# Performance work log

Hardware: AMD Instinct MI355X
Metric: run time of the kernel (lower is better)

The kernel has to match this reference:

```python
import jax, jax.numpy as jnp
import numpy as np

N_EMBD = 1024
N_HEAD = 16
HEAD_DIM = N_EMBD / N_HEAD  # used only for the attention scale, as in the source
LN_EPS = 1e-5


def _layernorm(x, g, b):
    mu = jnp.mean(x, axis=-1, keepdims=True)
    var = jnp.mean(jnp.square(x - mu), axis=-1, keepdims=True)
    return (x - mu) * jax.lax.rsqrt(var + LN_EPS) * g + b


def setup_inputs() -> dict:
    key = jax.random.key(0)
    ks = jax.random.split(key, 8)
    D = N_EMBD
    s = lambda n: 0.02  # GPT-style init scale
    x = jax.random.normal(ks[0], (4, 2048, D), dtype=jnp.float32)
    w_attn = jax.random.normal(ks[1], (D, 3 * D), dtype=jnp.float32) * s(D)
    b_attn = jnp.zeros((3 * D,), jnp.float32)
    w_proj = jax.random.normal(ks[2], (D, D), dtype=jnp.float32) * s(D)
    b_proj = jnp.zeros((D,), jnp.float32)
    ln1_g = jnp.ones((D,), jnp.float32)
    ln1_b = jnp.zeros((D,), jnp.float32)
    ln2_g = jnp.ones((D,), jnp.float32)
    ln2_b = jnp.zeros((D,), jnp.float32)
    w_fc = jax.random.normal(ks[3], (D, 4 * D), dtype=jnp.float32) * s(D)
    b_fc = jnp.zeros((4 * D,), jnp.float32)
    w_fc2 = jax.random.normal(ks[4], (4 * D, D), dtype=jnp.float32) * s(4 * D)
    b_fc2 = jnp.zeros((D,), jnp.float32)
    return {"x": x, "w_attn": w_attn, "b_attn": b_attn, "w_proj": w_proj,
            "b_proj": b_proj, "ln1_g": ln1_g, "ln1_b": ln1_b, "ln2_g": ln2_g,
            "ln2_b": ln2_b, "w_fc": w_fc, "b_fc": b_fc, "w_fc2": w_fc2,
            "b_fc2": b_fc2}


def reference(x, w_attn, b_attn, w_proj, b_proj, ln1_g, ln1_b, ln2_g, ln2_b,
              w_fc, b_fc, w_fc2, b_fc2):
    B, T, D = x.shape
    # --- attention branch (pre-LN) ---
    h = _layernorm(x, ln1_g, ln1_b)
    qkv = h @ w_attn + b_attn                     # [B,T,3D]
    q, k, v = jnp.split(qkv, 3, axis=-1)
    scale = 1.0 / np.sqrt(HEAD_DIM).astype(np.float32)
    att = jnp.einsum('btd,bsd->bts', q, k) * scale  # full-dim scores [B,T,T]
    causal = jnp.tril(jnp.ones((T, T), dtype=bool))
    att = jnp.where(causal[None, :, :], att, -jnp.inf)
    att = jax.nn.softmax(att, axis=-1)
    y = jnp.einsum('bts,bsd->btd', att, v)
    y = y @ w_proj + b_proj
    x = x + y
    # --- MLP branch (pre-LN) ---
    h = _layernorm(x, ln2_g, ln2_b)
    h = jax.nn.gelu(h @ w_fc + b_fc, approximate=True)
    h = h @ w_fc2 + b_fc2
    return x + h
```

## Files before the change

kernel.cpp:

```cpp
#include <hip/hip_runtime.h>
#include <math.h>


typedef unsigned short u16;
typedef __attribute__((ext_vector_type(8))) short bf16x8;
typedef __attribute__((ext_vector_type(8))) unsigned short u16x8;
typedef __attribute__((ext_vector_type(4))) float f32x4;

#define DEV __device__ __forceinline__

#define GLOAD_LDS16(gp, lp)                                                     \
    __builtin_amdgcn_global_load_lds(                                           \
        (const __attribute__((address_space(1))) void*)(gp),                    \
        (__attribute__((address_space(3))) void*)(lp), 16, 0, 0)

DEV float bf2f(u16 h) {
    union { unsigned u; float f; } t; t.u = ((unsigned)h) << 16; return t.f;
}
DEV u16 f2bf(float f) {
    union { unsigned u; float f; } t; t.f = f;
    unsigned u = t.u;
    return (u16)((u + 0x7FFFu + ((u >> 16) & 1u)) >> 16);
}
DEV float loadIn(const void* p, long i, int isbf) {
    return isbf ? bf2f(((const u16*)p)[i]) : ((const float*)p)[i];
}
DEV float gelu_fast(float x) {
    float u = 1.5957691216057308f * (x + 0.044715f * x * x * x);
    return x * __builtin_amdgcn_rcpf(1.0f + __expf(-u));
}

DEV float waveSum(float v) {
    #pragma unroll
    for (int o = 32; o > 0; o >>= 1) v += __shfl_down(v, o, 64);
    return v;
}
DEV float waveMax(float v) {
    #pragma unroll
    for (int o = 32; o > 0; o >>= 1) v = fmaxf(v, __shfl_down(v, o, 64));
    return v;
}

template <bool IS_MAX>
DEV float blockReduce(float v) {
    __shared__ float tmp[5];
    __syncthreads();
    v = IS_MAX ? waveMax(v) : waveSum(v);
    int lane = threadIdx.x & 63, w = threadIdx.x >> 6;
    if (lane == 0) tmp[w] = v;
    __syncthreads();
    if (threadIdx.x == 0) {
        float r = tmp[0];
        for (int i = 1; i < 4; i++) r = IS_MAX ? fmaxf(r, tmp[i]) : (r + tmp[i]);
        tmp[4] = r;
    }
    __syncthreads();
    return tmp[4];
}

__global__ void detect_dtype(const u16* __restrict__ xr, int* __restrict__ flag) {
    const int tid = threadIdx.x;
    int cnt = 0;
    #pragma unroll
    for (int i = 0; i < 16; i++) {
        unsigned u = xr[2 * (tid + 256 * i)];
        unsigned e = (u >> 7) & 0xFF;
        cnt += (e >= 100 && e <= 140) ? 1 : 0;
    }
    __shared__ int sh[4];
    #pragma unroll
    for (int o = 32; o > 0; o >>= 1) cnt += __shfl_down(cnt, o, 64);
    if ((tid & 63) == 0) sh[tid >> 6] = cnt;
    __syncthreads();
    if (tid == 0) flag[0] = (sh[0] + sh[1] + sh[2] + sh[3] > 2048) ? 1 : 0;
}

template <bool RAW_IN>
__global__ void ln_kernel(const void* __restrict__ x, const void* __restrict__ g,
                          const void* __restrict__ b, u16* __restrict__ out,
                          const int* __restrict__ flagp) {
    const int isbf = *flagp;
    const int inbf = RAW_IN ? isbf : 1;
    const long base = (long)blockIdx.x * 1024;
    const int tid = threadIdx.x;
    float v[4];
    #pragma unroll
    for (int j = 0; j < 4; j++) v[j] = loadIn(x, base + tid + 256 * j, inbf);
    float mu = blockReduce<false>(v[0] + v[1] + v[2] + v[3]) * (1.0f / 1024.0f);
    float d[4], sq = 0.f;
    #pragma unroll
    for (int j = 0; j < 4; j++) { d[j] = v[j] - mu; sq += d[j] * d[j]; }
    float var = blockReduce<false>(sq) * (1.0f / 1024.0f);
    float rstd = rsqrtf(var + 1e-5f);
    #pragma unroll
    for (int j = 0; j < 4; j++) {
        int c = tid + 256 * j;
        out[base + c] = f2bf(d[j] * rstd * loadIn(g, c, isbf) + loadIn(b, c, isbf));
    }
}

__global__ void transpose_to_bf16(const void* __restrict__ in, int ldin, long inBatch,
                                  u16* __restrict__ out, int ldout, long outBatch,
                                  const int* __restrict__ flagp) {
    __shared__ u16 tile[32][33];
    const int isbf = flagp ? *flagp : 1;
    const long ibase = (long)blockIdx.z * inBatch;
    out += (long)blockIdx.z * outBatch;
    const int bc = blockIdx.x * 32, br = blockIdx.y * 32;
    const int tx = threadIdx.x & 31, ty = threadIdx.x >> 5;
    #pragma unroll
    for (int i = 0; i < 32; i += 8)
        tile[ty + i][tx] = f2bf(loadIn(in, ibase + (long)(br + ty + i) * ldin + bc + tx, isbf));
    __syncthreads();
    #pragma unroll
    for (int i = 0; i < 32; i += 8)
        out[(long)(bc + ty + i) * ldout + br + tx] = tile[tx][ty + i];
}

template <int MODE, int CAUSAL, int TM>
__global__ __launch_bounds__(256) void gemm_mf(
        const u16* __restrict__ A, int lda, long aBatch,
        const u16* __restrict__ Bt, int ldb, long bBatch,
        const void* __restrict__ bias,
        void* __restrict__ Cv, int ldc, long cBatch,
        const void* __restrict__ res,
        float scale, const int* __restrict__ flagp, int K) {
    constexpr int FI = TM / 32;
    const int m0 = blockIdx.y * TM, n0 = blockIdx.x * 128;
    if (CAUSAL == 1 && n0 > m0 + TM - 1) return;
    __shared__ __align__(16) u16 sA[TM * 32];
    __shared__ __align__(16) u16 sB[128 * 32];
    const int bz = blockIdx.z;
    A  += (long)bz * aBatch + (long)m0 * lda;
    Bt += (long)bz * bBatch + (long)n0 * ldb;
    const int tid = threadIdx.x;
    const int wave = tid >> 6, lane = tid & 63;
    const int quad = lane >> 4, l16 = lane & 15;
    const int wr = (wave >> 1) * (TM / 2), wc = (wave & 1) * 64;

    const int c0 = tid;
    const int r0 = c0 >> 2;
    const int qs = (c0 & 3) ^ ((r0 >> 1) & 3);
    const u16* ag = A  + (long)r0 * lda + qs * 8;
    const u16* bg = Bt + (long)r0 * ldb + qs * 8;
    u16* sAd = sA + c0 * 8;
    u16* sBd = sB + c0 * 8;
    const long aStep = (long)64 * lda, bStep = (long)64 * ldb;

    f32x4 acc[FI][4];
    #pragma unroll
    for (int i = 0; i < FI; i++)
        #pragma unroll
        for (int j = 0; j < 4; j++)
            acc[i][j] = f32x4{0.f, 0.f, 0.f, 0.f};

    int Keff = K;
    if (CAUSAL == 2) Keff = min(K, m0 + TM);

    const int qa = quad ^ ((l16 >> 1) & 3);

    for (int k0 = 0; k0 < Keff; k0 += 32) {
        __syncthreads();
        GLOAD_LDS16(ag + k0, sAd);
        if (TM == 128) GLOAD_LDS16(ag + k0 + aStep, sAd + 2048);
        GLOAD_LDS16(bg + k0,         sBd);
        GLOAD_LDS16(bg + k0 + bStep, sBd + 2048);
        __syncthreads();
        bf16x8 af[FI], bfv[4];
        #pragma unroll
        for (int i = 0; i < FI; i++)
            af[i]  = *reinterpret_cast<const bf16x8*>(&sA[(wr + 16 * i + l16) * 32 + qa * 8]);
        #pragma unroll
        for (int j = 0; j < 4; j++)
            bfv[j] = *reinterpret_cast<const bf16x8*>(&sB[(wc + 16 * j + l16) * 32 + qa * 8]);
        #pragma unroll
        for (int i = 0; i < FI; i++)
            #pragma unroll
            for (int j = 0; j < 4; j++)
                acc[i][j] = __builtin_amdgcn_mfma_f32_16x16x32_bf16(
                    af[i], bfv[j], acc[i][j], 0, 0, 0);
    }

    const int isbf = (MODE == 0 || MODE == 3 || MODE == 4 || MODE == 5) ? *flagp : 1;
    #pragma unroll
    for (int i = 0; i < FI; i++) {
        #pragma unroll
        for (int j = 0; j < 4; j++) {
            #pragma unroll
            for (int r = 0; r < 4; r++) {
                const int row = m0 + wr + 16 * i + quad * 4 + r;
                const int col = n0 + wc + 16 * j + l16;
                const long idx = (long)bz * cBatch + (long)row * ldc + col;
                float v = acc[i][j][r];
                if (MODE == 1) {
                    reinterpret_cast<u16*>(Cv)[idx] = f2bf(v * scale);
                } else {
                    if (MODE != 2) v += loadIn(bias, col, isbf);
                    if (MODE == 4) v = gelu_fast(v);
                    if (MODE == 3) v += loadIn(res, (long)row * ldc + col, isbf);
                    if (MODE == 5) v += bf2f(((const u16*)res)[(long)row * ldc + col]);
                    if (MODE == 5 && !isbf)
                        reinterpret_cast<float*>(Cv)[idx] = v;
                    else
                        reinterpret_cast<u16*>(Cv)[idx] = f2bf(v);
                }
            }
        }
    }
}

__global__ void softmax_causal(const u16* __restrict__ S, u16* __restrict__ P) {
    const long row = blockIdx.x;
    const int t = (int)(row & 2047);
    const u16* sr = S + row * 2048;
    u16* pr = P + row * 2048;
    const int tid = threadIdx.x;
    const int s0 = tid * 8;
    float v[8];
    float mx = -INFINITY;
    if (s0 <= t) {
        u16x8 raw = *reinterpret_cast<const u16x8*>(sr + s0);
        #pragma unroll
        for (int i = 0; i < 8; i++) {
            float x = bf2f(raw[i]);
            v[i] = (s0 + i <= t) ? x : -INFINITY;
            mx = fmaxf(mx, v[i]);
        }
    } else {
        #pragma unroll
        for (int i = 0; i < 8; i++) v[i] = -INFINITY;
    }
    mx = blockReduce<true>(mx);
    float sum = 0.f;
    #pragma unroll
    for (int i = 0; i < 8; i++) {
        float e = (v[i] == -INFINITY) ? 0.0f : __expf(v[i] - mx);
        v[i] = e;
        sum += e;
    }
    sum = blockReduce<false>(sum);
    float inv = 1.0f / sum;
    if (s0 <= (t | 63)) {
        u16x8 o;
        #pragma unroll
        for (int i = 0; i < 8; i++) o[i] = f2bf(v[i] * inv);
        *reinterpret_cast<u16x8*>(pr + s0) = o;
    }
}

extern "C" void kernel_launch(void* const* d_in, const int* in_sizes, int n_in,
                              void* d_out, int out_size, void* d_ws, size_t ws_size,
                              hipStream_t stream) {
    const void* x      = d_in[0];
    const void* w_attn = d_in[1];
    const void* b_attn = d_in[2];
    const void* w_proj = d_in[3];
    const void* b_proj = d_in[4];
    const void* ln1_g  = d_in[5];
    const void* ln1_b  = d_in[6];
    const void* ln2_g  = d_in[7];
    const void* ln2_b  = d_in[8];
    const void* w_fc   = d_in[9];
    const void* b_fc   = d_in[10];
    const void* w_fc2  = d_in[11];
    const void* b_fc2  = d_in[12];

    char* ws = (char*)d_ws;
    u16*   hbuf   = (u16*)(ws);
    u16*   qkv    = (u16*)(ws + 16777216);
    u16*   S      = (u16*)(ws + 67108864);
    u16*   wattnT = (u16*)(ws + 134217728);
    u16*   wprojT = wattnT + 3072 * 1024;
    u16*   wfcT   = wprojT + 1024 * 1024;
    u16*   wfc2T  = wfcT + 4096 * 1024;
    u16*   vT     = wfc2T + 1024 * 4096;
    int*   flag   = (int*)(ws + 176160768);
    u16*   probs  = qkv;
    u16*   x1     = qkv + 16777216;

    detect_dtype<<<1, 256, 0, stream>>>((const u16*)x, flag);

    transpose_to_bf16<<<dim3(96, 32, 1),  256, 0, stream>>>(w_attn, 3072, 0, wattnT, 1024, 0, flag);
    transpose_to_bf16<<<dim3(32, 32, 1),  256, 0, stream>>>(w_proj, 1024, 0, wprojT, 1024, 0, flag);
    transpose_to_bf16<<<dim3(128, 32, 1), 256, 0, stream>>>(w_fc,   4096, 0, wfcT,   1024, 0, flag);
    transpose_to_bf16<<<dim3(32, 128, 1), 256, 0, stream>>>(w_fc2,  1024, 0, wfc2T,  4096, 0, flag);

    ln_kernel<true><<<8192, 256, 0, stream>>>(x, ln1_g, ln1_b, hbuf, flag);

    gemm_mf<0, 0, 128><<<dim3(24, 64, 1), 256, 0, stream>>>(
        hbuf, 1024, 0, wattnT, 1024, 0, b_attn, qkv, 3072, 0, nullptr, 0.f, flag, 1024);

    transpose_to_bf16<<<dim3(32, 64, 4), 256, 0, stream>>>(
        qkv + 2048, 3072, (long)2048 * 3072, vT, 2048, (long)1024 * 2048, nullptr);

    gemm_mf<1, 1, 64><<<dim3(16, 32, 4), 256, 0, stream>>>(
        qkv, 3072, (long)2048 * 3072, qkv + 1024, 3072, (long)2048 * 3072,
        nullptr, S, 2048, (long)2048 * 2048, nullptr, 0.125f, flag, 1024);

    softmax_causal<<<8192, 256, 0, stream>>>(S, probs);

    gemm_mf<2, 2, 64><<<dim3(8, 32, 4), 256, 0, stream>>>(
        probs, 2048, (long)2048 * 2048, vT, 2048, (long)1024 * 2048,
        nullptr, hbuf, 1024, (long)2048 * 1024, nullptr, 0.f, flag, 2048);

    gemm_mf<3, 0, 64><<<dim3(8, 128, 1), 256, 0, stream>>>(
        hbuf, 1024, 0, wprojT, 1024, 0, b_proj, x1, 1024, 0, x, 0.f, flag, 1024);

    ln_kernel<false><<<8192, 256, 0, stream>>>(x1, ln2_g, ln2_b, hbuf, flag);

    gemm_mf<4, 0, 128><<<dim3(32, 64, 1), 256, 0, stream>>>(
        hbuf, 1024, 0, wfcT, 1024, 0, b_fc, S, 4096, 0, nullptr, 0.f, flag, 1024);

    gemm_mf<5, 0, 128><<<dim3(8, 64, 1), 256, 0, stream>>>(
        S, 4096, 0, wfc2T, 4096, 0, b_fc2, d_out, 1024, 0, x1, 0.f, flag, 4096);
}
```

Baseline: 689.0 us.

## Add 256x256-tile 8-wave pipelined GEMM for QKV and MLP projections

Introduces a new bf16 MFMA GEMM kernel with 256x256 output tiles, 512 threads (8 waves), XOR-swizzled LDS, double-buffered direct global-to-LDS loads split into four phases interleaved with compute, and an XCD-aware block swizzle. It replaces the previous 128-tile GEMM for the QKV, FC and FC2 projections, aiming at more data reuse per tile and overlap of loads with MFMA work. The cost is larger LDS use (128 KB per block) and heavy register pressure from 32 accumulators per thread. Grids are also much smaller (e.g. 128 blocks for FC2), which may leave part of the GPU idle.

After: 696.6 us. About the same (+1.1%).

```diff
diff --git a/kernel.cpp b/kernel.cpp
--- a/kernel.cpp
+++ b/kernel.cpp
@@ -209,6 +209,138 @@
     }
 }
 
+template <int MODE>
+__global__ __launch_bounds__(512, 2) void gemm_8ph(
+        const u16* __restrict__ A, int lda,
+        const u16* __restrict__ Bt, int ldb,
+        const void* __restrict__ bias,
+        void* __restrict__ Cv, int ldc,
+        const void* __restrict__ res,
+        const int* __restrict__ flagp, int K) {
+    __shared__ __align__(16) u16 sA[2][256 * 64];
+    __shared__ __align__(16) u16 sB[2][256 * 64];
+
+    const int gx  = gridDim.x;
+    const int nwg = gx * gridDim.y;
+    const int fid = blockIdx.y * gx + blockIdx.x;
+    const int swz = (fid & 7) * (nwg >> 3) + (fid >> 3);
+    const int m0 = (swz / gx) * 256, n0 = (swz % gx) * 256;
+
+    const int tid  = threadIdx.x;
+    const int lane = tid & 63, wv = tid >> 6;
+    const int wm = wv >> 2, wn = wv & 3;
+    const int l16 = lane & 15, quad = lane >> 4;
+    const int xg = l16 & 7;
+
+    const int rq   = tid >> 3;
+    const int gsrc = ((tid & 7) ^ (rq & 7)) * 8;
+    const int gdst = (tid & 7) * 8;
+    const int rAb  = (rq < 32) ? rq : 96 + rq;
+
+    const int NT = K >> 6;
+
+#define STAGE8(t_, q_) do {                                                      \
+        const int sl_ = (t_) & 1;                                                \
+        const int k0_ = (t_) << 6;                                               \
+        const int ra_ = ((q_) << 5) + rAb;                                       \
+        GLOAD_LDS16(A + (long)(m0 + ra_) * lda + k0_ + gsrc,                     \
+                    &sA[sl_][ra_ * 64 + gdst]);                                  \
+        const int rb_ = ((q_) << 6) + rq;                                        \
+        GLOAD_LDS16(Bt + (long)(n0 + rb_) * ldb + k0_ + gsrc,                    \
+                    &sB[sl_][rb_ * 64 + gdst]);                                  \
+    } while (0)
+
+#define PBAR8() do { __builtin_amdgcn_sched_barrier(0);                          \
+        asm volatile("s_barrier" ::: "memory");                                  \
+        __builtin_amdgcn_sched_barrier(0); } while (0)
+
+#define WVM8(n_) do { __builtin_amdgcn_sched_barrier(0);                         \
+        asm volatile("s_waitcnt vmcnt(" #n_ ")" ::: "memory");                   \
+        __builtin_amdgcn_sched_barrier(0); } while (0)
+
+    f32x4 acc[8][4];
+    #pragma unroll
+    for (int i = 0; i < 8; i++)
+        #pragma unroll
+        for (int j = 0; j < 4; j++) acc[i][j] = f32x4{0.f, 0.f, 0.f, 0.f};
+
+    STAGE8(0, 0); STAGE8(0, 1); STAGE8(0, 2); STAGE8(0, 3);
+    WVM8(4);
+    STAGE8(1, 0); STAGE8(1, 1); STAGE8(1, 2);
+    WVM8(6);
+    PBAR8();
+
+    for (int u = 0; u < NT; ++u) {
+        const int su = u & 1;
+        bf16x8 bfr[4][2];
+        #pragma unroll
+        for (int q = 0; q < 4; ++q) {
+            bf16x8 af[2][2];
+            #pragma unroll
+            for (int f = 0; f < 2; ++f)
+                #pragma unroll
+                for (int s = 0; s < 2; ++s)
+                    af[f][s] = *reinterpret_cast<const bf16x8*>(
+                        &sA[su][(wm * 128 + (2 * q + f) * 16 + l16) * 64 +
+                                (((s * 4 + quad) ^ xg) * 8)]);
+            if (q == 0) {
+                #pragma unroll
+                for (int j = 0; j < 4; ++j)
+                    #pragma unroll
+                    for (int s = 0; s < 2; ++s)
+                        bfr[j][s] = *reinterpret_cast<const bf16x8*>(
+                            &sB[su][(wn * 64 + j * 16 + l16) * 64 +
+                                    (((s * 4 + quad) ^ xg) * 8)]);
+            }
+            if (q == 0) { if (u + 1 < NT) STAGE8(u + 1, 3); }
+            else        { if (u + 2 < NT) STAGE8(u + 2, q - 1); }
+            PBAR8();
+            __builtin_amdgcn_s_setprio(1);
+            #pragma unroll
+            for (int f = 0; f < 2; ++f)
+                #pragma unroll
+                for (int j = 0; j < 4; ++j) {
+                    acc[2 * q + f][j] = __builtin_amdgcn_mfma_f32_16x16x32_bf16(
+                        af[f][0], bfr[j][0], acc[2 * q + f][j], 0, 0, 0);
+                    acc[2 * q + f][j] = __builtin_amdgcn_mfma_f32_16x16x32_bf16(
+                        af[f][1], bfr[j][1], acc[2 * q + f][j], 0, 0, 0);
+                }
+            __builtin_amdgcn_s_setprio(0);
+            if (q < 3) {
+                PBAR8();
+            } else if (u + 1 < NT) {
+                if (u + 2 < NT) { WVM8(6); } else { WVM8(0); }
+                PBAR8();
+            }
+        }
+    }
+
+    const int isbf = *flagp;
+    #pragma unroll
+    for (int mi = 0; mi < 8; ++mi) {
+        #pragma unroll
+        for (int j = 0; j < 4; ++j) {
+            #pragma unroll
+            for (int r = 0; r < 4; ++r) {
+                const int row = m0 + wm * 128 + mi * 16 + quad * 4 + r;
+                const int col = n0 + wn * 64 + j * 16 + l16;
+                const long idx = (long)row * ldc + col;
+                float v = acc[mi][j][r];
+                v += loadIn(bias, col, isbf);
+                if (MODE == 4) v = gelu_fast(v);
+                if (MODE == 5) v += bf2f(((const u16*)res)[idx]);
+                if (MODE == 5 && !isbf)
+                    reinterpret_cast<float*>(Cv)[idx] = v;
+                else
+                    reinterpret_cast<u16*>(Cv)[idx] = f2bf(v);
+            }
+        }
+    }
+#undef STAGE8
+#undef PBAR8
+#undef WVM8
+}
+
 __global__ void softmax_causal(const u16* __restrict__ S, u16* __restrict__ P) {
     const long row = blockIdx.x;
     const int t = (int)(row & 2047);
@@ -287,8 +419,8 @@
 
     ln_kernel<true><<<8192, 256, 0, stream>>>(x, ln1_g, ln1_b, hbuf, flag);
 
-    gemm_mf<0, 0, 128><<<dim3(24, 64, 1), 256, 0, stream>>>(
-        hbuf, 1024, 0, wattnT, 1024, 0, b_attn, qkv, 3072, 0, nullptr, 0.f, flag, 1024);
+    gemm_8ph<0><<<dim3(12, 32, 1), 512, 0, stream>>>(
+        hbuf, 1024, wattnT, 1024, b_attn, qkv, 3072, nullptr, flag, 1024);
 
     transpose_to_bf16<<<dim3(32, 64, 4), 256, 0, stream>>>(
         qkv + 2048, 3072, (long)2048 * 3072, vT, 2048, (long)1024 * 2048, nullptr);
@@ -308,9 +440,9 @@
 
     ln_kernel<false><<<8192, 256, 0, stream>>>(x1, ln2_g, ln2_b, hbuf, flag);
 
-    gemm_mf<4, 0, 128><<<dim3(32, 64, 1), 256, 0, stream>>>(
-        hbuf, 1024, 0, wfcT, 1024, 0, b_fc, S, 4096, 0, nullptr, 0.f, flag, 1024);
-
-    gemm_mf<5, 0, 128><<<dim3(8, 64, 1), 256, 0, stream>>>(
-        S, 4096, 0, wfc2T, 4096, 0, b_fc2, d_out, 1024, 0, x1, 0.f, flag, 4096);
-}
+    gemm_8ph<4><<<dim3(16, 32, 1), 512, 0, stream>>>(
+        hbuf, 1024, wfcT, 1024, b_fc, S, 4096, nullptr, flag, 1024);
+
+    gemm_8ph<5><<<dim3(4, 32, 1), 512, 0, stream>>>(
+        S, 4096, wfc2T, 4096, b_fc2, d_out, 1024, x1, flag, 4096);
+}
```

## Replace GEMM with 256x256 double-buffered eight-phase pipelined MFMA kernel

Applied to the files above, without the earlier changes.

Swaps the simple 128/64-row tile GEMM for a 512-thread kernel using 256x256 tiles and BK=64. Global-to-LDS loads are double-buffered and split into four quarter stages, interleaved with MFMA phases through explicit waitcnt and barriers. The kernel also adds a triangular block enumeration for the causal score GEMM and an XCD-style block swizzle for the dense GEMMs. Softmax zero-fill is widened to 256 columns to match the larger causal tile. The aim is more data reuse and overlap of memory with MFMA work. The cost is much higher register and LDS use, fewer blocks for the smaller GEMMs, and more causal waste per tile.

Result: no change. 686.5 us (-0.4%).

```diff
diff --git a/kernel.cpp b/kernel.cpp
--- a/kernel.cpp
+++ b/kernel.cpp
@@ -13,6 +13,12 @@
     __builtin_amdgcn_global_load_lds(                                           \
         (const __attribute__((address_space(1))) void*)(gp),                    \
         (__attribute__((address_space(3))) void*)(lp), 16, 0, 0)
+
+#define DSR128(dst_, p_)                                                        \
+    asm volatile("ds_read_b128 %0, %1"                                          \
+                 : "=v"(dst_)                                                   \
+                 : "v"((unsigned)(unsigned long long)                           \
+                       (__attribute__((address_space(3))) const void*)(p_)))
 
 DEV float bf2f(u16 h) {
     union { unsigned u; float f; } t; t.u = ((unsigned)h) << 16; return t.f;
@@ -117,85 +123,174 @@
         out[(long)(bc + ty + i) * ldout + br + tx] = tile[tx][ty + i];
 }
 
-template <int MODE, int CAUSAL, int TM>
-__global__ __launch_bounds__(256) void gemm_mf(
+template <int MODE, int CAUSAL>
+__global__ __launch_bounds__(512, 2) void gemm_8ph(
         const u16* __restrict__ A, int lda, long aBatch,
         const u16* __restrict__ Bt, int ldb, long bBatch,
         const void* __restrict__ bias,
         void* __restrict__ Cv, int ldc, long cBatch,
         const void* __restrict__ res,
         float scale, const int* __restrict__ flagp, int K) {
-    constexpr int FI = TM / 32;
-    const int m0 = blockIdx.y * TM, n0 = blockIdx.x * 128;
-    if (CAUSAL == 1 && n0 > m0 + TM - 1) return;
-    __shared__ __align__(16) u16 sA[TM * 32];
-    __shared__ __align__(16) u16 sB[128 * 32];
+    __shared__ __align__(16) u16 sA[2][256 * 64];
+    __shared__ __align__(16) u16 sB[2][256 * 64];
+
+    int m0, n0;
+    if (CAUSAL == 1) {
+        const int bx = blockIdx.x;
+        int ti = (int)((sqrtf(8.0f * bx + 1.0f) - 1.0f) * 0.5f);
+        while ((ti + 1) * (ti + 2) / 2 <= bx) ++ti;
+        while (ti * (ti + 1) / 2 > bx) --ti;
+        m0 = ti * 256;
+        n0 = (bx - ti * (ti + 1) / 2) * 256;
+    } else if (CAUSAL == 2) {
+        m0 = blockIdx.y * 256;
+        n0 = blockIdx.x * 256;
+    } else {
+        const int gx  = gridDim.x;
+        const int nwg = gx * gridDim.y;
+        const int fid = blockIdx.y * gx + blockIdx.x;
+        const int swz = (fid & 7) * (nwg >> 3) + (fid >> 3);
+        m0 = (swz / gx) * 256;
+        n0 = (swz % gx) * 256;
+    }
     const int bz = blockIdx.z;
-    A  += (long)bz * aBatch + (long)m0 * lda;
-    Bt += (long)bz * bBatch + (long)n0 * ldb;
-    const int tid = threadIdx.x;
-    const int wave = tid >> 6, lane = tid & 63;
-    const int quad = lane >> 4, l16 = lane & 15;
-    const int wr = (wave >> 1) * (TM / 2), wc = (wave & 1) * 64;
-
-    const int c0 = tid;
-    const int r0 = c0 >> 2;
-    const int qs = (c0 & 3) ^ ((r0 >> 1) & 3);
-    const u16* ag = A  + (long)r0 * lda + qs * 8;
-    const u16* bg = Bt + (long)r0 * ldb + qs * 8;
-    u16* sAd = sA + c0 * 8;
-    u16* sBd = sB + c0 * 8;
-    const long aStep = (long)64 * lda, bStep = (long)64 * ldb;
-
-    f32x4 acc[FI][4];
-    #pragma unroll
-    for (int i = 0; i < FI; i++)
+    A  += (long)bz * aBatch;
+    Bt += (long)bz * bBatch;
+
+    const int tid  = threadIdx.x;
+    const int lane = tid & 63, wv = tid >> 6;
+    const int wm = wv >> 2, wn = wv & 3;
+    const int l16 = lane & 15, quad = lane >> 4;
+    const int xg = l16 & 7;
+
+    const int rq   = tid >> 3;
+    const int gsrc = ((tid & 7) ^ (rq & 7)) * 8;
+    const int gdst = (tid & 7) * 8;
+    const int rAb  = (rq < 32) ? rq : 96 + rq;
+
+    int NT = K >> 6;
+    if (CAUSAL == 2) NT = min(K, m0 + 256) >> 6;
+
+#define STAGE8(t_, q_) do {                                                      \
+        const int sl_ = (t_) & 1;                                                \
+        const int k0_ = (t_) << 6;                                               \
+        const int ra_ = ((q_) << 5) + rAb;                                       \
+        GLOAD_LDS16(A + (long)(m0 + ra_) * lda + k0_ + gsrc,                     \
+                    &sA[sl_][ra_ * 64 + gdst]);                                  \
+        const int rb_ = ((q_) << 6) + rq;                                        \
+        GLOAD_LDS16(Bt + (long)(n0 + rb_) * ldb + k0_ + gsrc,                    \
+                    &sB[sl_][rb_ * 64 + gdst]);                                  \
+    } while (0)
+
+#define PBAR8() do { __builtin_amdgcn_sched_barrier(0);                          \
+        asm volatile("s_barrier" ::: "memory");                                  \
+        __builtin_amdgcn_sched_barrier(0); } while (0)
+
+#define WVM8(n_) do { __builtin_amdgcn_sched_barrier(0);                         \
+        asm volatile("s_waitcnt vmcnt(" #n_ ")" ::: "memory");                   \
+        __builtin_amdgcn_sched_barrier(0); } while (0)
+
+#define WLGKM(n_) do { __builtin_amdgcn_sched_barrier(0);                        \
+        asm volatile("s_waitcnt lgkmcnt(" #n_ ")" ::: "memory");                 \
+        __builtin_amdgcn_sched_barrier(0); } while (0)
+
+#define RD_A(buf_, qn_, sl_) do {                                                \
+        DSR128(buf_[0][0], &sA[sl_][(wm * 128 + (2 * (qn_) + 0) * 16 + l16) * 64 \
+                                    + (((0 * 4 + quad) ^ xg) * 8)]);             \
+        DSR128(buf_[0][1], &sA[sl_][(wm * 128 + (2 * (qn_) + 0) * 16 + l16) * 64 \
+                                    + (((1 * 4 + quad) ^ xg) * 8)]);             \
+        DSR128(buf_[1][0], &sA[sl_][(wm * 128 + (2 * (qn_) + 1) * 16 + l16) * 64 \
+                                    + (((0 * 4 + quad) ^ xg) * 8)]);             \
+        DSR128(buf_[1][1], &sA[sl_][(wm * 128 + (2 * (qn_) + 1) * 16 + l16) * 64 \
+                                    + (((1 * 4 + quad) ^ xg) * 8)]);             \
+    } while (0)
+
+#define RD_B(sl_) do {                                                           \
+        DSR128(bC[0][0], &sB[sl_][(wn * 64 + 0 * 16 + l16) * 64 + (((0 * 4 + quad) ^ xg) * 8)]); \
+        DSR128(bC[0][1], &sB[sl_][(wn * 64 + 0 * 16 + l16) * 64 + (((1 * 4 + quad) ^ xg) * 8)]); \
+        DSR128(bC[1][0], &sB[sl_][(wn * 64 + 1 * 16 + l16) * 64 + (((0 * 4 + quad) ^ xg) * 8)]); \
+        DSR128(bC[1][1], &sB[sl_][(wn * 64 + 1 * 16 + l16) * 64 + (((1 * 4 + quad) ^ xg) * 8)]); \
+        DSR128(bC[2][0], &sB[sl_][(wn * 64 + 2 * 16 + l16) * 64 + (((0 * 4 + quad) ^ xg) * 8)]); \
+        DSR128(bC[2][1], &sB[sl_][(wn * 64 + 2 * 16 + l16) * 64 + (((1 * 4 + quad) ^ xg) * 8)]); \
+        DSR128(bC[3][0], &sB[sl_][(wn * 64 + 3 * 16 + l16) * 64 + (((0 * 4 + quad) ^ xg) * 8)]); \
+        DSR128(bC[3][1], &sB[sl_][(wn * 64 + 3 * 16 + l16) * 64 + (((1 * 4 + quad) ^ xg) * 8)]); \
+    } while (0)
+
+#define MFMA_PH(q_, A_) do {                                                     \
+        __builtin_amdgcn_s_setprio(1);                                           \
+        _Pragma("unroll")                                                        \
+        for (int f_ = 0; f_ < 2; ++f_)                                           \
+            _Pragma("unroll")                                                    \
+            for (int j_ = 0; j_ < 4; ++j_) {                                     \
+                acc[2 * (q_) + f_][j_] = __builtin_amdgcn_mfma_f32_16x16x32_bf16(\
+                    A_[f_][0], bC[j_][0], acc[2 * (q_) + f_][j_], 0, 0, 0);      \
+                acc[2 * (q_) + f_][j_] = __builtin_amdgcn_mfma_f32_16x16x32_bf16(\
+                    A_[f_][1], bC[j_][1], acc[2 * (q_) + f_][j_], 0, 0, 0);      \
+            }                                                                    \
+        __builtin_amdgcn_s_setprio(0);                                           \
+    } while (0)
+
+    f32x4 acc[8][4];
+    #pragma unroll
+    for (int i = 0; i < 8; i++)
         #pragma unroll
-        for (int j = 0; j < 4; j++)
-            acc[i][j] = f32x4{0.f, 0.f, 0.f, 0.f};
-
-    int Keff = K;
-    if (CAUSAL == 2) Keff = min(K, m0 + TM);
-
-    const int qa = quad ^ ((l16 >> 1) & 3);
-
-    for (int k0 = 0; k0 < Keff; k0 += 32) {
-        __syncthreads();
-        GLOAD_LDS16(ag + k0, sAd);
-        if (TM == 128) GLOAD_LDS16(ag + k0 + aStep, sAd + 2048);
-        GLOAD_LDS16(bg + k0,         sBd);
-        GLOAD_LDS16(bg + k0 + bStep, sBd + 2048);
-        __syncthreads();
-        bf16x8 af[FI], bfv[4];
+        for (int j = 0; j < 4; j++) acc[i][j] = f32x4{0.f, 0.f, 0.f, 0.f};
+
+    bf16x8 afA[2][2], afB[2][2], bC[4][2];
+
+    STAGE8(0, 0); STAGE8(0, 1); STAGE8(0, 2); STAGE8(0, 3);
+    STAGE8(1, 0); STAGE8(1, 1); STAGE8(1, 2);
+    WVM8(6);
+    PBAR8();
+    RD_A(afA, 0, 0);
+
+    for (int u = 0; u < NT; ++u) {
+        const int su = u & 1, sn = su ^ 1;
+        if (u + 1 < NT) STAGE8(u + 1, 3);
+        __builtin_amdgcn_sched_barrier(0);
+        RD_B(su);
+        RD_A(afB, 1, su);
+        WLGKM(4);
+        MFMA_PH(0, afA);
+        PBAR8();
+        if (u + 2 < NT) STAGE8(u + 2, 0);
+        __builtin_amdgcn_sched_barrier(0);
+        RD_A(afA, 2, su);
+        WLGKM(4);
+        MFMA_PH(1, afB);
+        PBAR8();
+        if (u + 2 < NT) STAGE8(u + 2, 1);
+        __builtin_amdgcn_sched_barrier(0);
+        RD_A(afB, 3, su);
+        WLGKM(4);
+        MFMA_PH(2, afA);
+        PBAR8();
+        if (u + 2 < NT) { STAGE8(u + 2, 2); WVM8(6); } else { WVM8(0); }
+        PBAR8();
+        RD_A(afA, 0, sn);
+        WLGKM(4);
+        MFMA_PH(3, afB);
+        PBAR8();
+    }
+    WLGKM(0);
+
+    const int isbf = (MODE == 0 || MODE == 3 || MODE == 4 || MODE == 5) ? *flagp : 1;
+    #pragma unroll
+    for (int mi = 0; mi < 8; ++mi) {
         #pragma unroll
-        for (int i = 0; i < FI; i++)
-            af[i]  = *reinterpret_cast<const bf16x8*>(&sA[(wr + 16 * i + l16) * 32 + qa * 8]);
-        #pragma unroll
-        for (int j = 0; j < 4; j++)
-            bfv[j] = *reinterpret_cast<const bf16x8*>(&sB[(wc + 16 * j + l16) * 32 + qa * 8]);
-        #pragma unroll
-        for (int i = 0; i < FI; i++)
+        for (int j = 0; j < 4; ++j) {
             #pragma unroll
-            for (int j = 0; j < 4; j++)
-                acc[i][j] = __builtin_amdgcn_mfma_f32_16x16x32_bf16(
-                    af[i], bfv[j], acc[i][j], 0, 0, 0);
-    }
-
-    const int isbf = (MODE == 0 || MODE == 3 || MODE == 4 || MODE == 5) ? *flagp : 1;
-    #pragma unroll
-    for (int i = 0; i < FI; i++) {
-        #pragma unroll
-        for (int j = 0; j < 4; j++) {
-            #pragma unroll
-            for (int r = 0; r < 4; r++) {
-                const int row = m0 + wr + 16 * i + quad * 4 + r;
-                const int col = n0 + wc + 16 * j + l16;
+            for (int r = 0; r < 4; ++r) {
+                const int row = m0 + wm * 128 + mi * 16 + quad * 4 + r;
+                const int col = n0 + wn * 64 + j * 16 + l16;
                 const long idx = (long)bz * cBatch + (long)row * ldc + col;
-                float v = acc[i][j][r];
+                float v = acc[mi][j][r];
                 if (MODE == 1) {
                     reinterpret_cast<u16*>(Cv)[idx] = f2bf(v * scale);
+                } else if (MODE == 2) {
+                    reinterpret_cast<u16*>(Cv)[idx] = f2bf(v);
                 } else {
-                    if (MODE != 2) v += loadIn(bias, col, isbf);
+                    v += loadIn(bias, col, isbf);
                     if (MODE == 4) v = gelu_fast(v);
                     if (MODE == 3) v += loadIn(res, (long)row * ldc + col, isbf);
                     if (MODE == 5) v += bf2f(((const u16*)res)[(long)row * ldc + col]);
@@ -207,6 +302,13 @@
             }
         }
     }
+#undef STAGE8
+#undef PBAR8
+#undef WVM8
+#undef WLGKM
+#undef RD_A
+#undef RD_B
+#undef MFMA_PH
 }
 
 __global__ void softmax_causal(const u16* __restrict__ S, u16* __restrict__ P) {
@@ -240,7 +342,7 @@
     }
     sum = blockReduce<false>(sum);
     float inv = 1.0f / sum;
-    if (s0 <= (t | 63)) {
+    if (s0 <= (t | 255)) {
         u16x8 o;
         #pragma unroll
         for (int i = 0; i < 8; i++) o[i] = f2bf(v[i] * inv);
@@ -287,30 +389,30 @@
 
     ln_kernel<true><<<8192, 256, 0, stream>>>(x, ln1_g, ln1_b, hbuf, flag);
 
-    gemm_mf<0, 0, 128><<<dim3(24, 64, 1), 256, 0, stream>>>(
+    gemm_8ph<0, 0><<<dim3(12, 32, 1), 512, 0, stream>>>(
         hbuf, 1024, 0, wattnT, 1024, 0, b_attn, qkv, 3072, 0, nullptr, 0.f, flag, 1024);
 
     transpose_to_bf16<<<dim3(32, 64, 4), 256, 0, stream>>>(
         qkv + 2048, 3072, (long)2048 * 3072, vT, 2048, (long)1024 * 2048, nullptr);
 
-    gemm_mf<1, 1, 64><<<dim3(16, 32, 4), 256, 0, stream>>>(
+    gemm_8ph<1, 1><<<dim3(36, 1, 4), 512, 0, stream>>>(
         qkv, 3072, (long)2048 * 3072, qkv + 1024, 3072, (long)2048 * 3072,
         nullptr, S, 2048, (long)2048 * 2048, nullptr, 0.125f, flag, 1024);
 
     softmax_causal<<<8192, 256, 0, stream>>>(S, probs);
 
-    gemm_mf<2, 2, 64><<<dim3(8, 32, 4), 256, 0, stream>>>(
+    gemm_8ph<2, 2><<<dim3(4, 8, 4), 512, 0, stream>>>(
         probs, 2048, (long)2048 * 2048, vT, 2048, (long)1024 * 2048,
         nullptr, hbuf, 1024, (long)2048 * 1024, nullptr, 0.f, flag, 2048);
 
-    gemm_mf<3, 0, 64><<<dim3(8, 128, 1), 256, 0, stream>>>(
+    gemm_8ph<3, 0><<<dim3(4, 32, 1), 512, 0, stream>>>(
         hbuf, 1024, 0, wprojT, 1024, 0, b_proj, x1, 1024, 0, x, 0.f, flag, 1024);
 
     ln_kernel<false><<<8192, 256, 0, stream>>>(x1, ln2_g, ln2_b, hbuf, flag);
 
-    gemm_mf<4, 0, 128><<<dim3(32, 64, 1), 256, 0, stream>>>(
+    gemm_8ph<4, 0><<<dim3(16, 32, 1), 512, 0, stream>>>(
         hbuf, 1024, 0, wfcT, 1024, 0, b_fc, S, 4096, 0, nullptr, 0.f, flag, 1024);
 
-    gemm_mf<5, 0, 128><<<dim3(8, 64, 1), 256, 0, stream>>>(
+    gemm_8ph<5, 0><<<dim3(4, 32, 1), 512, 0, stream>>>(
         S, 4096, 0, wfc2T, 4096, 0, b_fc2, d_out, 1024, 0, x1, 0.f, flag, 4096);
 }
```
